# Kernel tuning notes

Measured on AMD Instinct MI355X. Metric: run time of the kernel, lower is better.

The kernel has to match this reference:

```python
import jax, jax.numpy as jnp
import numpy as np
from jax.scipy.special import erf

NSPOTS = 20000
PATTERNS = 6
ROISIZE = 16
SIGMA = 1.5           # PSF gaussian sigma in pixels
ITERATIONS = 50
LAMBDA = 100.0        # fixed Levenberg damping (lambda_ in the torch module)
I_MIN, I_MAX = 1.0, 1e6     # param_range row 0 (intensity)
BG_MIN, BG_MAX = 1.0, 1e3   # param_range row 1 (background)
MU_EPS = 1e-9


def _gauss_psf(xy):
    """Pixel-integrated 2D Gaussian PSF, unit intensity, zero bg. xy: [N,2] -> [N,R,R]."""
    pix = jnp.arange(ROISIZE, dtype=xy.dtype)
    c = 1.0 / (np.sqrt(2.0) * SIGMA)

    def edge(center):  # per-axis integrated gaussian over unit pixels
        d = pix[None, :] - center[:, None]
        return 0.5 * (erf((d + 1.0) * c) - erf(d * c))

    Ex = edge(xy[:, 0])  # [N,R]
    Ey = edge(xy[:, 1])  # [N,R]
    return Ey[:, :, None] * Ex[:, None, :]  # rows = y, cols = x


def setup_inputs() -> dict:
    key = jax.random.key(0)
    k1, k2, k3, k4, k5 = jax.random.split(key, 5)
    xy = ROISIZE / 2 + jax.random.normal(k1, (NSPOTS, 2), dtype=jnp.float32)
    I = 500.0 + 1000.0 * jax.random.uniform(k2, (NSPOTS,), dtype=jnp.float32)
    bg = 2.0 + 8.0 * jax.random.uniform(k3, (NSPOTS,), dtype=jnp.float32)
    # params layout: [x, y, I, bg, total-intensity estimate used as LM init]
    params = jnp.stack([xy[:, 0], xy[:, 1], I, bg, I], axis=1)
    # synthetic photon-count data: per-pattern modulated spot + bg + sqrt-noise, clipped >= 0
    psf = _gauss_psf(xy)
    mod = 0.5 + 0.5 * jax.random.uniform(k4, (NSPOTS, PATTERNS, 1, 1), dtype=jnp.float32)
    mu_true = (I[:, None, None, None] / PATTERNS) * mod * psf[:, None] + bg[:, None, None, None] / PATTERNS
    noise = jax.random.normal(k5, mu_true.shape, dtype=jnp.float32) * jnp.sqrt(mu_true)
    data = jnp.maximum(mu_true + noise, 0.0)
    return {"params": params, "data": data}


def reference(params, data):
    nspots, patterns, R, _ = data.shape
    N = nspots * patterns

    # psf_model with I forced to 1 and bg to 0 -> normalized PSF image per spot
    psf = _gauss_psf(params[:, :2])                 # [nspots,R,R]
    psf = jnp.repeat(psf, patterns, axis=0)         # repeat_interleave -> [N,R,R]
    smp = data.reshape(N, R, R)

    # initial_ibg: I0 = params[:,4]/patterns (final overwrite in torch code), bg0 = 0
    I0 = jnp.repeat(params[:, 4] / patterns, patterns)
    init = jnp.stack([I0, jnp.zeros_like(I0)], axis=1)  # [N,2]

    s = lambda a: a.sum((1, 2))  # reduce over ROI pixels

    @jax.checkpoint
    def step(cur, _):
        I, bg = cur[:, 0], cur[:, 1]
        mu = jnp.clip(I[:, None, None] * psf + bg[:, None, None], MU_EPS, None)
        af = smp / (mu * mu)          # Fisher weight  smp/mu^2
        df = smp / mu - 1.0           # Poisson LL gradient weight
        # 2x2 LM system, diagonal Levenberg damping with fixed lambda
        a00 = s(af * psf * psf) + LAMBDA
        a01 = s(af * psf)
        a11 = s(af) + LAMBDA
        b0 = s(df * psf)
        b1 = s(df)
        det = a00 * a11 - a01 * a01
        dI = (a11 * b0 - a01 * b1) / det
        dbg = (a00 * b1 - a01 * b0) / det
        I = jnp.clip(I + dI, I_MIN, I_MAX)
        bg = jnp.clip(bg + dbg, BG_MIN, BG_MAX)
        return jnp.stack([I, bg], axis=1), None

    estim, _ = jax.lax.scan(step, init, None, length=ITERATIONS)  # [N,2]

    # CRLB from Poisson Fisher info with jac = [psf, 1]
    I, bg = estim[:, 0], estim[:, 1]
    mu = I[:, None, None] * psf + bg[:, None, None]
    inv = 1.0 / jnp.clip(mu, MU_EPS, None)
    F00 = s(psf * psf * inv)
    F01 = s(psf * inv)
    F11 = s(inv)
    detF = F00 * F11 - F01 * F01
    crlb = jnp.sqrt(jnp.stack([F11 / detF, F00 / detF], axis=1))  # sqrt(diag(F^-1))

    chisq = (((smp - mu) ** 2) / (mu + 0.01)).sum((1, 2))

    # pack (estim, crlb, chisq) -> [nspots, patterns, 5]
    return jnp.concatenate([
        estim.reshape(nspots, patterns, 2),
        crlb.reshape(nspots, patterns, 2),
        chisq.reshape(nspots, patterns, 1),
    ], axis=-1)
```

## Files before the change

### kernel.cpp

```cpp
#include <hip/hip_runtime.h>
#include <math.h>

#define PATTERNS 6
#define ITERS 50
#define LAMBDA_ 100.0f
#define CST 0.47140452079103173f

typedef float v2f __attribute__((ext_vector_type(2)));

__device__ __forceinline__ float grpsum8(float x) {
    x += __int_as_float(__builtin_amdgcn_ds_swizzle(__float_as_int(x), 0x041F));
    x += __int_as_float(__builtin_amdgcn_ds_swizzle(__float_as_int(x), 0x081F));
    x += __int_as_float(__builtin_amdgcn_ds_swizzle(__float_as_int(x), 0x101F));
    return x;
}

#define PAIRS(X) X(0) X(1) X(2) X(3) X(4) X(5) X(6) X(7) \
                 X(8) X(9) X(10) X(11) X(12) X(13) X(14) X(15)

template<int K>
__device__ __forceinline__ void compose_window(
    float Ua0, float Ua1, float Ua2,
    float b0a, float b1a, float rda, float Ia, float bga,
    float& I, float& bg)
{
    float a00 = Ua2 + LAMBDA_;
    float a01 = Ua1;
    float a11 = Ua0 + LAMBDA_;
    float r0I = b0a - fmaf(Ua2, I - Ia, Ua1 * (bg - bga));
    float r0B = b1a - fmaf(Ua1, I - Ia, Ua0 * (bg - bga));
    float lr = LAMBDA_ * rda;
    float G00 = lr * a11;
    float G01 = -(lr * a01);
    float G11 = lr * a00;
    float Pd00 = G00, Pd01 = G01, Pd11 = G11;
    float Sd00 = 1.0f, Sd01 = 0.0f, Sd11 = 1.0f;
    float Pa00 = 1.0f, Pa01 = 0.0f, Pa11 = 1.0f;
    float Sa00 = 0.0f, Sa01 = 0.0f, Sa11 = 0.0f;
    float T00, T01, T11;
#define SYMMUL(p,q,r_, s_,t_,u_) \
    T00 = fmaf(p, s_, q * t_); \
    T01 = fmaf(p, t_, q * u_); \
    T11 = fmaf(q, t_, r_ * u_);
#pragma unroll
    for (int j = 0; j < 6; ++j) {
        if ((K >> j) & 1) {
            SYMMUL(Pa00, Pa01, Pa11, Sd00, Sd01, Sd11)
            Sa00 += T00; Sa01 += T01; Sa11 += T11;
            SYMMUL(Pa00, Pa01, Pa11, Pd00, Pd01, Pd11)
            Pa00 = T00; Pa01 = T01; Pa11 = T11;
        }
        if ((K >> (j + 1)) != 0) {
            SYMMUL(Pd00, Pd01, Pd11, Sd00, Sd01, Sd11)
            Sd00 += T00; Sd01 += T01; Sd11 += T11;
            SYMMUL(Pd00, Pd01, Pd11, Pd00, Pd01, Pd11)
            Pd00 = T00; Pd01 = T01; Pd11 = T11;
        }
    }
#undef SYMMUL
    float w0 = fmaf(Sa00, r0I, Sa01 * r0B);
    float w1 = fmaf(Sa01, r0I, Sa11 * r0B);
    float I2  = I  + rda * fmaf(a11, w0, -(a01 * w1));
    float bg2 = bg + rda * fmaf(a00, w1, -(a01 * w0));
    float gam = rda * fmaf(a11, Ua2, -(a01 * Ua1));
    float c0 = b0a - Ua1 * (1.0f - bga);
    float c1 = b1a - Ua0 * (1.0f - bga);
    float beta = rda * fmaf(a11, c0, -(a01 * c1));
    float Iinf = Ia + beta * __builtin_amdgcn_rcpf(gam);
    float t = 1.0f - gam;
    float rho = 1.0f, tp = t;
#pragma unroll
    for (int j = 0; j < 6; ++j) {
        if ((K >> j) & 1) rho *= tp;
        if ((K >> (j + 1)) != 0) tp *= tp;
    }
    float I1d = Iinf + rho * (I - Iinf);
    bool interior = (bg2 >= 1.0f);
    I  = interior ? I2 : I1d;
    bg = interior ? bg2 : 1.0f;
    I  = fminf(fmaxf(I, 1.0f), 1000000.0f);
    bg = fminf(bg, 1000.0f);
}

__global__ __launch_bounds__(256, 3) void intensity_kernel(
    const float* __restrict__ params,
    const float* __restrict__ data,
    float* __restrict__ out,
    int njobs)
{
    const int tid = blockIdx.x * 256 + threadIdx.x;
    const int job = tid >> 3;
    const int sub = tid & 7;
    if (job >= njobs) return;
    const int spot = job / PATTERNS;

    const float x = params[spot * 5 + 0];
    const float y = params[spot * 5 + 1];
    float I = params[spot * 5 + 4] * (1.0f / PATTERNS);
    float bg = 0.0f;

#define DECLV(k) v2f g##k, s##k;
    PAIRS(DECLV)
#undef DECLV

    {
        const float4* dp = reinterpret_cast<const float4*>(data + (size_t)job * 256 + sub * 32);
        float4 v;
        v = dp[0]; s0  = (v2f){v.x, v.y}; s1  = (v2f){v.z, v.w};
        v = dp[1]; s2  = (v2f){v.x, v.y}; s3  = (v2f){v.z, v.w};
        v = dp[2]; s4  = (v2f){v.x, v.y}; s5  = (v2f){v.z, v.w};
        v = dp[3]; s6  = (v2f){v.x, v.y}; s7  = (v2f){v.z, v.w};
        v = dp[4]; s8  = (v2f){v.x, v.y}; s9  = (v2f){v.z, v.w};
        v = dp[5]; s10 = (v2f){v.x, v.y}; s11 = (v2f){v.z, v.w};
        v = dp[6]; s12 = (v2f){v.x, v.y}; s13 = (v2f){v.z, v.w};
        v = dp[7]; s14 = (v2f){v.x, v.y}; s15 = (v2f){v.z, v.w};
    }

    {
        const float r0f = (float)(2 * sub);
        const float ey_a = erff((r0f - y) * CST);
        const float ey_b = erff((r0f + 1.0f - y) * CST);
        const float ey_c = erff((r0f + 2.0f - y) * CST);
        const float eyl0 = 0.5f * (ey_b - ey_a);
        const float eyl1 = 0.5f * (ey_c - ey_b);

        const float c0 = (float)(2 * sub);
        const float ea = erff((c0 - x) * CST);
        const float eb = erff((c0 + 1.0f - x) * CST);
        const float ec = erff((c0 + 2.0f - x) * CST);
        const float exa = 0.5f * (eb - ea);
        const float exb = 0.5f * (ec - eb);

        const int wl = threadIdx.x & 63;
        const int gb4 = (wl & 0x38) << 2;

        {
            int idx; float eA, eB;
#define MKG2(k, lo, hi) \
            idx = gb4 + (k << 2); \
            eA = __int_as_float(__builtin_amdgcn_ds_bpermute(idx, __float_as_int(exa))); \
            eB = __int_as_float(__builtin_amdgcn_ds_bpermute(idx, __float_as_int(exb))); \
            lo = (v2f){eyl0 * eA, eyl0 * eB}; \
            hi = (v2f){eyl1 * eA, eyl1 * eB};
            MKG2(0, g0, g8)
            MKG2(1, g1, g9)
            MKG2(2, g2, g10)
            MKG2(3, g3, g11)
            MKG2(4, g4, g12)
            MKG2(5, g5, g13)
            MKG2(6, g6, g14)
            MKG2(7, g7, g15)
#undef MKG2
        }
    }

    float spsf, Ss;
    {
        v2f sp = (v2f){0.0f, 0.0f};
        v2f ssum = (v2f){0.0f, 0.0f};
#define ADDG(k) sp += g##k; ssum += s##k;
        PAIRS(ADDG)
#undef ADDG
        spsf = grpsum8(sp[0] + sp[1]);
        Ss   = grpsum8(ssum[0] + ssum[1]);
    }

    float Ua0 = 0.0f, Ua1 = 0.0f, Ua2 = 0.0f;
    float b0a = 0.0f, b1a = 0.0f, rda = 0.0f, Ia = 0.0f, bga = 0.0f;

#define BODY(k) { \
        v2f mu = g##k * I + bge; \
        v2f r; \
        r[0] = __builtin_amdgcn_rcpf(mu[0]); \
        r[1] = __builtin_amdgcn_rcpf(mu[1]); \
        v2f t = s##k * r; \
        P1 += t; \
        P2 = t * r + P2; }

#define FULL_ITER { \
        const float bge = bg + 1e-9f; \
        v2f P1 = (v2f){0.0f, 0.0f}, P2 = (v2f){0.0f, 0.0f}; \
        PAIRS(BODY) \
        float T1 = grpsum8(P1[0] + P1[1]); \
        float T2 = grpsum8(P2[0] + P2[1]); \
        float rI = __builtin_amdgcn_rcpf(I); \
        float U0 = T2; \
        float U1 = (T1 - bge * T2) * rI; \
        float U2 = fmaf(bge, fmaf(bge, T2, -(T1 + T1)), Ss) * (rI * rI); \
        float b0 = fmaf(-bge, T1, Ss) * rI - spsf; \
        float b1 = T1 - 256.0f; \
        float a00 = U2 + LAMBDA_; \
        float a01 = U1; \
        float a11 = U0 + LAMBDA_; \
        float det = fmaf(a00, a11, -(a01 * a01)); \
        float rd = __builtin_amdgcn_rcpf(det); \
        Ua0 = U0; Ua1 = U1; Ua2 = U2; \
        b0a = b0; b1a = b1; rda = rd; Ia = I; bga = bg; \
        float dI  = fmaf(a11, b0, -(a01 * b1)) * rd; \
        float dbg = fmaf(a00, b1, -(a01 * b0)) * rd; \
        I  = fminf(fmaxf(I + dI, 1.0f), 1000000.0f); \
        bg = fminf(fmaxf(bg + dbg, 1.0f), 1000.0f); }

    FULL_ITER
    FULL_ITER
    FULL_ITER
    compose_window<22>(Ua0, Ua1, Ua2, b0a, b1a, rda, Ia, bga, I, bg);
    FULL_ITER
    compose_window<24>(Ua0, Ua1, Ua2, b0a, b1a, rda, Ia, bga, I, bg);

#undef BODY
#undef FULL_ITER

    float V1 = 0.0f, chis = 0.0f;
#define EPI(k) { \
        v2f mu = g##k * I + bg; \
        v2f inv; \
        inv[0] = __builtin_amdgcn_rcpf(mu[0]); \
        inv[1] = __builtin_amdgcn_rcpf(mu[1]); \
        v2f d  = s##k - mu; \
        v2f ic; \
        ic[0] = fmaf(-0.01f * inv[0], inv[0], inv[0]); \
        ic[1] = fmaf(-0.01f * inv[1], inv[1], inv[1]); \
        V1 += inv[0] + inv[1]; \
        chis += d[0] * d[0] * ic[0] + d[1] * d[1] * ic[1]; }
    PAIRS(EPI)
#undef EPI
    {
        float t0 = __int_as_float(__builtin_amdgcn_ds_swizzle(__float_as_int(V1), 0x041F));
        float t1 = __int_as_float(__builtin_amdgcn_ds_swizzle(__float_as_int(chis), 0x041F));
        V1 += t0; chis += t1;
        t0 = __int_as_float(__builtin_amdgcn_ds_swizzle(__float_as_int(V1), 0x081F));
        t1 = __int_as_float(__builtin_amdgcn_ds_swizzle(__float_as_int(chis), 0x081F));
        V1 += t0; chis += t1;
        t0 = __int_as_float(__builtin_amdgcn_ds_swizzle(__float_as_int(V1), 0x101F));
        t1 = __int_as_float(__builtin_amdgcn_ds_swizzle(__float_as_int(chis), 0x101F));
        V1 += t0; chis += t1;
    }

    if (sub == 0) {
        float rI = __builtin_amdgcn_rcpf(I);
        float F11 = V1;
        float F01 = fmaf(-bg, V1, 256.0f) * rI;
        float F00 = (fmaf(bg * bg, V1, I * spsf) - 256.0f * bg) * (rI * rI);
        float detF = fmaf(F00, F11, -(F01 * F01));
        float rdF = __builtin_amdgcn_rcpf(detF);
        float* o = out + (size_t)job * 5;
        o[0] = I;
        o[1] = bg;
        o[2] = sqrtf(F11 * rdF);
        o[3] = sqrtf(F00 * rdF);
        o[4] = chis;
    }
}

extern "C" void kernel_launch(void* const* d_in, const int* in_sizes, int n_in,
                              void* d_out, int out_size, void* d_ws, size_t ws_size,
                              hipStream_t stream) {
    const float* params = (const float*)d_in[0];
    const float* data   = (const float*)d_in[1];
    float* out = (float*)d_out;
    int nspots = in_sizes[0] / 5;
    int njobs = nspots * PATTERNS;
    long long nthreads = (long long)njobs * 8;
    int blocks = (int)((nthreads + 255) / 256);
    intensity_kernel<<<dim3(blocks), dim3(256), 0, stream>>>(params, data, out, njobs);
}
```

Measured before the change: 43.19 us.

## Split each fit job across 16 lanes, one image row per lane

```diff
diff --git a/kernel.cpp b/kernel.cpp
--- a/kernel.cpp
+++ b/kernel.cpp
@@ -8,15 +8,15 @@
 
 typedef float v2f __attribute__((ext_vector_type(2)));
 
-__device__ __forceinline__ float grpsum8(float x) {
+__device__ __forceinline__ float grpsum16(float x) {
     x += __int_as_float(__builtin_amdgcn_ds_swizzle(__float_as_int(x), 0x041F));
     x += __int_as_float(__builtin_amdgcn_ds_swizzle(__float_as_int(x), 0x081F));
     x += __int_as_float(__builtin_amdgcn_ds_swizzle(__float_as_int(x), 0x101F));
+    x += __int_as_float(__builtin_amdgcn_ds_swizzle(__float_as_int(x), 0x201F));
     return x;
 }
 
-#define PAIRS(X) X(0) X(1) X(2) X(3) X(4) X(5) X(6) X(7) \
-                 X(8) X(9) X(10) X(11) X(12) X(13) X(14) X(15)
+#define PAIRS(X) X(0) X(1) X(2) X(3) X(4) X(5) X(6) X(7)
 
 template<int K>
 __device__ __forceinline__ void compose_window(
@@ -82,15 +82,15 @@
     bg = fminf(bg, 1000.0f);
 }
 
-__global__ __launch_bounds__(256, 3) void intensity_kernel(
+__global__ __launch_bounds__(256, 4) void intensity_kernel(
     const float* __restrict__ params,
     const float* __restrict__ data,
     float* __restrict__ out,
     int njobs)
 {
     const int tid = blockIdx.x * 256 + threadIdx.x;
-    const int job = tid >> 3;
-    const int sub = tid & 7;
+    const int job = tid >> 4;
+    const int sub = tid & 15;
     if (job >= njobs) return;
     const int spot = job / PATTERNS;
 
@@ -104,54 +104,31 @@
 #undef DECLV
 
     {
-        const float4* dp = reinterpret_cast<const float4*>(data + (size_t)job * 256 + sub * 32);
+        const float4* dp = reinterpret_cast<const float4*>(data + (size_t)job * 256 + sub * 16);
         float4 v;
-        v = dp[0]; s0  = (v2f){v.x, v.y}; s1  = (v2f){v.z, v.w};
-        v = dp[1]; s2  = (v2f){v.x, v.y}; s3  = (v2f){v.z, v.w};
-        v = dp[2]; s4  = (v2f){v.x, v.y}; s5  = (v2f){v.z, v.w};
-        v = dp[3]; s6  = (v2f){v.x, v.y}; s7  = (v2f){v.z, v.w};
-        v = dp[4]; s8  = (v2f){v.x, v.y}; s9  = (v2f){v.z, v.w};
-        v = dp[5]; s10 = (v2f){v.x, v.y}; s11 = (v2f){v.z, v.w};
-        v = dp[6]; s12 = (v2f){v.x, v.y}; s13 = (v2f){v.z, v.w};
-        v = dp[7]; s14 = (v2f){v.x, v.y}; s15 = (v2f){v.z, v.w};
-    }
-
-    {
-        const float r0f = (float)(2 * sub);
-        const float ey_a = erff((r0f - y) * CST);
-        const float ey_b = erff((r0f + 1.0f - y) * CST);
-        const float ey_c = erff((r0f + 2.0f - y) * CST);
-        const float eyl0 = 0.5f * (ey_b - ey_a);
-        const float eyl1 = 0.5f * (ey_c - ey_b);
-
-        const float c0 = (float)(2 * sub);
-        const float ea = erff((c0 - x) * CST);
-        const float eb = erff((c0 + 1.0f - x) * CST);
-        const float ec = erff((c0 + 2.0f - x) * CST);
-        const float exa = 0.5f * (eb - ea);
-        const float exb = 0.5f * (ec - eb);
+        v = dp[0]; s0 = (v2f){v.x, v.y}; s1 = (v2f){v.z, v.w};
+        v = dp[1]; s2 = (v2f){v.x, v.y}; s3 = (v2f){v.z, v.w};
+        v = dp[2]; s4 = (v2f){v.x, v.y}; s5 = (v2f){v.z, v.w};
+        v = dp[3]; s6 = (v2f){v.x, v.y}; s7 = (v2f){v.z, v.w};
+    }
+
+    {
+        const float fy = (float)sub - y;
+        const float eyl = 0.5f * (erff((fy + 1.0f) * CST) - erff(fy * CST));
+        const float fx = (float)sub - x;
+        const float exa = 0.5f * (erff((fx + 1.0f) * CST) - erff(fx * CST));
 
         const int wl = threadIdx.x & 63;
-        const int gb4 = (wl & 0x38) << 2;
-
-        {
-            int idx; float eA, eB;
-#define MKG2(k, lo, hi) \
-            idx = gb4 + (k << 2); \
-            eA = __int_as_float(__builtin_amdgcn_ds_bpermute(idx, __float_as_int(exa))); \
-            eB = __int_as_float(__builtin_amdgcn_ds_bpermute(idx, __float_as_int(exb))); \
-            lo = (v2f){eyl0 * eA, eyl0 * eB}; \
-            hi = (v2f){eyl1 * eA, eyl1 * eB};
-            MKG2(0, g0, g8)
-            MKG2(1, g1, g9)
-            MKG2(2, g2, g10)
-            MKG2(3, g3, g11)
-            MKG2(4, g4, g12)
-            MKG2(5, g5, g13)
-            MKG2(6, g6, g14)
-            MKG2(7, g7, g15)
-#undef MKG2
-        }
+        const int gb4 = (wl & 0x30) << 2;
+
+        int idx; float eA, eB;
+#define MKG(k) \
+        idx = gb4 + ((2 * k) << 2); \
+        eA = __int_as_float(__builtin_amdgcn_ds_bpermute(idx,     __float_as_int(exa))); \
+        eB = __int_as_float(__builtin_amdgcn_ds_bpermute(idx + 4, __float_as_int(exa))); \
+        g##k = (v2f){eyl * eA, eyl * eB};
+        MKG(0) MKG(1) MKG(2) MKG(3) MKG(4) MKG(5) MKG(6) MKG(7)
+#undef MKG
     }
 
     float spsf, Ss;
@@ -161,8 +138,8 @@
 #define ADDG(k) sp += g##k; ssum += s##k;
         PAIRS(ADDG)
 #undef ADDG
-        spsf = grpsum8(sp[0] + sp[1]);
-        Ss   = grpsum8(ssum[0] + ssum[1]);
+        spsf = grpsum16(sp[0] + sp[1]);
+        Ss   = grpsum16(ssum[0] + ssum[1]);
     }
 
     float Ua0 = 0.0f, Ua1 = 0.0f, Ua2 = 0.0f;
@@ -181,8 +158,8 @@
         const float bge = bg + 1e-9f; \
         v2f P1 = (v2f){0.0f, 0.0f}, P2 = (v2f){0.0f, 0.0f}; \
         PAIRS(BODY) \
-        float T1 = grpsum8(P1[0] + P1[1]); \
-        float T2 = grpsum8(P2[0] + P2[1]); \
+        float T1 = grpsum16(P1[0] + P1[1]); \
+        float T2 = grpsum16(P2[0] + P2[1]); \
         float rI = __builtin_amdgcn_rcpf(I); \
         float U0 = T2; \
         float U1 = (T1 - bge * T2) * rI; \
@@ -235,6 +212,9 @@
         t0 = __int_as_float(__builtin_amdgcn_ds_swizzle(__float_as_int(V1), 0x101F));
         t1 = __int_as_float(__builtin_amdgcn_ds_swizzle(__float_as_int(chis), 0x101F));
         V1 += t0; chis += t1;
+        t0 = __int_as_float(__builtin_amdgcn_ds_swizzle(__float_as_int(V1), 0x201F));
+        t1 = __int_as_float(__builtin_amdgcn_ds_swizzle(__float_as_int(chis), 0x201F));
+        V1 += t0; chis += t1;
     }
 
     if (sub == 0) {
@@ -261,7 +241,7 @@
     float* out = (float*)d_out;
     int nspots = in_sizes[0] / 5;
     int njobs = nspots * PATTERNS;
-    long long nthreads = (long long)njobs * 8;
+    long long nthreads = (long long)njobs * 16;
     int blocks = (int)((nthreads + 255) / 256);
     intensity_kernel<<<dim3(blocks), dim3(256), 0, stream>>>(params, data, out, njobs);
 }
```

Result: slower. 53.56 us (+24.0%).

## Stage pixel data in LDS and factor PSF to cut registers, raise occupancy

Applied to the files above, without the earlier changes.

```diff
diff --git a/kernel.cpp b/kernel.cpp
--- a/kernel.cpp
+++ b/kernel.cpp
@@ -15,8 +15,7 @@
     return x;
 }
 
-#define PAIRS(X) X(0) X(1) X(2) X(3) X(4) X(5) X(6) X(7) \
-                 X(8) X(9) X(10) X(11) X(12) X(13) X(14) X(15)
+#define COLS(X) X(0) X(1) X(2) X(3) X(4) X(5) X(6) X(7)
 
 template<int K>
 __device__ __forceinline__ void compose_window(
@@ -82,47 +81,52 @@
     bg = fminf(bg, 1000.0f);
 }
 
-__global__ __launch_bounds__(256, 3) void intensity_kernel(
+__global__ __launch_bounds__(256, 5) void intensity_kernel(
     const float* __restrict__ params,
     const float* __restrict__ data,
     float* __restrict__ out,
     int njobs)
 {
-    const int tid = blockIdx.x * 256 + threadIdx.x;
+    __shared__ float slds[256 * 32];
+
+    const int t = threadIdx.x;
+    const int tid = blockIdx.x * 256 + t;
     const int job = tid >> 3;
     const int sub = tid & 7;
     if (job >= njobs) return;
     const int spot = job / PATTERNS;
 
+    const int laneB = (t << 7) ^ ((t & 15) << 3);
+#define SADDR(k) (*(v2f*)((char*)slds + (laneB ^ ((k) << 3))))
+
     const float x = params[spot * 5 + 0];
     const float y = params[spot * 5 + 1];
     float I = params[spot * 5 + 4] * (1.0f / PATTERNS);
     float bg = 0.0f;
 
-#define DECLV(k) v2f g##k, s##k;
-    PAIRS(DECLV)
-#undef DECLV
-
+    float Ss;
     {
         const float4* dp = reinterpret_cast<const float4*>(data + (size_t)job * 256 + sub * 32);
-        float4 v;
-        v = dp[0]; s0  = (v2f){v.x, v.y}; s1  = (v2f){v.z, v.w};
-        v = dp[1]; s2  = (v2f){v.x, v.y}; s3  = (v2f){v.z, v.w};
-        v = dp[2]; s4  = (v2f){v.x, v.y}; s5  = (v2f){v.z, v.w};
-        v = dp[3]; s6  = (v2f){v.x, v.y}; s7  = (v2f){v.z, v.w};
-        v = dp[4]; s8  = (v2f){v.x, v.y}; s9  = (v2f){v.z, v.w};
-        v = dp[5]; s10 = (v2f){v.x, v.y}; s11 = (v2f){v.z, v.w};
-        v = dp[6]; s12 = (v2f){v.x, v.y}; s13 = (v2f){v.z, v.w};
-        v = dp[7]; s14 = (v2f){v.x, v.y}; s15 = (v2f){v.z, v.w};
-    }
-
+        float ssum = 0.0f;
+#pragma unroll
+        for (int q = 0; q < 8; ++q) {
+            float4 v = dp[q];
+            ssum += (v.x + v.y) + (v.z + v.w);
+            SADDR(2 * q)     = (v2f){v.x, v.y};
+            SADDR(2 * q + 1) = (v2f){v.z, v.w};
+        }
+        Ss = grpsum8(ssum);
+    }
+
+    v2f ex0, ex1, ex2, ex3, ex4, ex5, ex6, ex7;
+    float eyl0, eyl1, spsf;
     {
         const float r0f = (float)(2 * sub);
         const float ey_a = erff((r0f - y) * CST);
         const float ey_b = erff((r0f + 1.0f - y) * CST);
         const float ey_c = erff((r0f + 2.0f - y) * CST);
-        const float eyl0 = 0.5f * (ey_b - ey_a);
-        const float eyl1 = 0.5f * (ey_c - ey_b);
+        eyl0 = 0.5f * (ey_b - ey_a);
+        eyl1 = 0.5f * (ey_c - ey_b);
 
         const float c0 = (float)(2 * sub);
         const float ea = erff((c0 - x) * CST);
@@ -131,56 +135,50 @@
         const float exa = 0.5f * (eb - ea);
         const float exb = 0.5f * (ec - eb);
 
-        const int wl = threadIdx.x & 63;
+        const int wl = t & 63;
         const int gb4 = (wl & 0x38) << 2;
 
-        {
-            int idx; float eA, eB;
-#define MKG2(k, lo, hi) \
-            idx = gb4 + (k << 2); \
-            eA = __int_as_float(__builtin_amdgcn_ds_bpermute(idx, __float_as_int(exa))); \
-            eB = __int_as_float(__builtin_amdgcn_ds_bpermute(idx, __float_as_int(exb))); \
-            lo = (v2f){eyl0 * eA, eyl0 * eB}; \
-            hi = (v2f){eyl1 * eA, eyl1 * eB};
-            MKG2(0, g0, g8)
-            MKG2(1, g1, g9)
-            MKG2(2, g2, g10)
-            MKG2(3, g3, g11)
-            MKG2(4, g4, g12)
-            MKG2(5, g5, g13)
-            MKG2(6, g6, g14)
-            MKG2(7, g7, g15)
-#undef MKG2
-        }
-    }
-
-    float spsf, Ss;
-    {
-        v2f sp = (v2f){0.0f, 0.0f};
-        v2f ssum = (v2f){0.0f, 0.0f};
-#define ADDG(k) sp += g##k; ssum += s##k;
-        PAIRS(ADDG)
-#undef ADDG
-        spsf = grpsum8(sp[0] + sp[1]);
-        Ss   = grpsum8(ssum[0] + ssum[1]);
+        int idx; float eA, eB;
+#define MKEX(k) \
+        idx = gb4 + ((k) << 2); \
+        eA = __int_as_float(__builtin_amdgcn_ds_bpermute(idx, __float_as_int(exa))); \
+        eB = __int_as_float(__builtin_amdgcn_ds_bpermute(idx, __float_as_int(exb))); \
+        ex##k = (v2f){eA, eB};
+        COLS(MKEX)
+#undef MKEX
+        v2f exs = ex0 + ex1 + ex2 + ex3 + ex4 + ex5 + ex6 + ex7;
+        spsf = (exs[0] + exs[1]) * grpsum8(eyl0 + eyl1);
     }
 
     float Ua0 = 0.0f, Ua1 = 0.0f, Ua2 = 0.0f;
     float b0a = 0.0f, b1a = 0.0f, rda = 0.0f, Ia = 0.0f, bga = 0.0f;
 
-#define BODY(k) { \
-        v2f mu = g##k * I + bge; \
+#define BODYA(k) { \
+        v2f s = SADDR(k); \
+        v2f mu = ex##k * IeyA + bge; \
         v2f r; \
         r[0] = __builtin_amdgcn_rcpf(mu[0]); \
         r[1] = __builtin_amdgcn_rcpf(mu[1]); \
-        v2f t = s##k * r; \
-        P1 += t; \
-        P2 = t * r + P2; }
+        v2f tt = s * r; \
+        P1 += tt; \
+        P2 = tt * r + P2; }
+#define BODYB(k) { \
+        v2f s = SADDR(8 + k); \
+        v2f mu = ex##k * IeyB + bge; \
+        v2f r; \
+        r[0] = __builtin_amdgcn_rcpf(mu[0]); \
+        r[1] = __builtin_amdgcn_rcpf(mu[1]); \
+        v2f tt = s * r; \
+        P1 += tt; \
+        P2 = tt * r + P2; }
 
 #define FULL_ITER { \
         const float bge = bg + 1e-9f; \
+        const float IeyA = I * eyl0; \
+        const float IeyB = I * eyl1; \
         v2f P1 = (v2f){0.0f, 0.0f}, P2 = (v2f){0.0f, 0.0f}; \
-        PAIRS(BODY) \
+        COLS(BODYA) \
+        COLS(BODYB) \
         float T1 = grpsum8(P1[0] + P1[1]); \
         float T2 = grpsum8(P2[0] + P2[1]); \
         float rI = __builtin_amdgcn_rcpf(I); \
@@ -208,23 +206,43 @@
     FULL_ITER
     compose_window<24>(Ua0, Ua1, Ua2, b0a, b1a, rda, Ia, bga, I, bg);
 
-#undef BODY
+#undef BODYA
+#undef BODYB
 #undef FULL_ITER
 
     float V1 = 0.0f, chis = 0.0f;
-#define EPI(k) { \
-        v2f mu = g##k * I + bg; \
+    {
+        const float IeyA = I * eyl0;
+        const float IeyB = I * eyl1;
+#define EPIA(k) { \
+        v2f s = SADDR(k); \
+        v2f mu = ex##k * IeyA + bg; \
         v2f inv; \
         inv[0] = __builtin_amdgcn_rcpf(mu[0]); \
         inv[1] = __builtin_amdgcn_rcpf(mu[1]); \
-        v2f d  = s##k - mu; \
+        v2f d  = s - mu; \
         v2f ic; \
         ic[0] = fmaf(-0.01f * inv[0], inv[0], inv[0]); \
         ic[1] = fmaf(-0.01f * inv[1], inv[1], inv[1]); \
         V1 += inv[0] + inv[1]; \
         chis += d[0] * d[0] * ic[0] + d[1] * d[1] * ic[1]; }
-    PAIRS(EPI)
-#undef EPI
+#define EPIB(k) { \
+        v2f s = SADDR(8 + k); \
+        v2f mu = ex##k * IeyB + bg; \
+        v2f inv; \
+        inv[0] = __builtin_amdgcn_rcpf(mu[0]); \
+        inv[1] = __builtin_amdgcn_rcpf(mu[1]); \
+        v2f d  = s - mu; \
+        v2f ic; \
+        ic[0] = fmaf(-0.01f * inv[0], inv[0], inv[0]); \
+        ic[1] = fmaf(-0.01f * inv[1], inv[1], inv[1]); \
+        V1 += inv[0] + inv[1]; \
+        chis += d[0] * d[0] * ic[0] + d[1] * d[1] * ic[1]; }
+        COLS(EPIA)
+        COLS(EPIB)
+#undef EPIA
+#undef EPIB
+    }
     {
         float t0 = __int_as_float(__builtin_amdgcn_ds_swizzle(__float_as_int(V1), 0x041F));
         float t1 = __int_as_float(__builtin_amdgcn_ds_swizzle(__float_as_int(chis), 0x041F));
@@ -251,6 +269,7 @@
         o[3] = sqrtf(F00 * rdF);
         o[4] = chis;
     }
+#undef SADDR
 }
 
 extern "C" void kernel_launch(void* const* d_in, const int* in_sizes, int n_in,
```

After: 44.05 us. No clear change (+2.0%).
